# Optimization experiments

Hardware: AMD Instinct MI355X
Metric: run time of the kernel (lower is better)

Reference implementation:

```python
import jax, jax.numpy as jnp
import numpy as np


def setup_inputs() -> dict:
    key = jax.random.key(0)
    k1, k2 = jax.random.split(key)
    N, D, C = 8192, 512, 100
    e = jax.random.normal(k1, (N, D), dtype=jnp.float32)
    y = jax.random.randint(k2, (N,), 0, C, dtype=jnp.int64)
    return {"e": e, "y": y}


def reference(e, y):
    # L2-normalize rows (matches e / sqrt(sum(e*e, dim=1, keepdim=True)))
    e_norm = e / jnp.sqrt(jnp.sum(e * e, axis=1, keepdims=True))
    # Pairwise cosine similarities [N, N]
    sim = e_norm @ e_norm.T
    N = e.shape[0]
    # Pairs (i1, i2) with i1 < i2 and y[i1] != y[i2]
    upper = jnp.triu(jnp.ones((N, N), dtype=bool), k=1)
    diff_label = y[:, None] != y[None, :]
    mask = (upper & diff_label).astype(sim.dtype)
    cnter = jnp.sum(mask)
    loss = jnp.sum(sim * mask)
    return loss / cnter
```

## Files before the change

kernel.cpp:

```cpp
#include <hip/hip_runtime.h>
#include <hip/hip_bf16.h>

constexpr int N = 8192;
constexpr int D = 512;
constexpr int C = 100;
constexpr int CAP = 256;
constexpr int SLICES = 4;
constexpr int SLICE_D = D / SLICES;
constexpr int CHUNKS = 4;

constexpr size_t OFF_CLASSSUM = 512;
constexpr size_t OFF_INVN     = OFF_CLASSSUM + (size_t)C * D * 4;
constexpr size_t OFF_LIST     = OFF_INVN + (size_t)N * 4;
constexpr size_t ZERO_BYTES   = OFF_CLASSSUM + (size_t)C * D * 4;

__global__ __launch_bounds__(256) void norm_kernel(
    const float* __restrict__ e,
    const int* __restrict__ y,
    float* __restrict__ invn,
    int* __restrict__ counts,
    int* __restrict__ list) {
  const int row  = (blockIdx.x * 256 + threadIdx.x) >> 6;
  const int lane = threadIdx.x & 63;
  if (row >= N) return;

  const float4* ep = reinterpret_cast<const float4*>(e + (size_t)row * D);
  const float4 a = ep[lane];
  const float4 b = ep[lane + 64];
  float ss = a.x * a.x + a.y * a.y + a.z * a.z + a.w * a.w
           + b.x * b.x + b.y * b.y + b.z * b.z + b.w * b.w;
  #pragma unroll
  for (int off = 32; off > 0; off >>= 1) ss += __shfl_xor(ss, off);

  if (lane == 0) {
    invn[row] = 1.0f / sqrtf(ss);
    const int c = y[row];
    const int pos = atomicAdd(counts + c, 1);
    if (pos < CAP) list[c * CAP + pos] = row;
  }
}

__global__ __launch_bounds__(128) void gather_kernel(
    const float* __restrict__ e,
    const float* __restrict__ invn,
    const int* __restrict__ counts,
    const int* __restrict__ list,
    float* __restrict__ classSum) {
  const int c   = blockIdx.x / (SLICES * CHUNKS);
  const int s   = (blockIdx.x / CHUNKS) % SLICES;
  const int h   = blockIdx.x % CHUNKS;
  const int tid = threadIdx.x;

  int n = counts[c];
  if (n > CAP) n = CAP;
  const int per = (n + CHUNKS - 1) / CHUNKS;
  const int k0  = h * per;
  int k1 = k0 + per;
  if (k1 > n) k1 = n;
  const int m = k1 - k0;
  if (m <= 0) return;

  __shared__ int   ls[CAP / CHUNKS];
  __shared__ float li[CAP / CHUNKS];
  if (tid < m) {
    const int r = list[c * CAP + k0 + tid];
    ls[tid] = r;
    li[tid] = invn[r];
  }
  __syncthreads();

  float acc = 0.0f;
  const float* base = e + s * SLICE_D + tid;
  #pragma unroll 4
  for (int k = 0; k < m; ++k) {
    acc += base[(size_t)ls[k] * D] * li[k];
  }

  atomicAdd(classSum + c * D + s * SLICE_D + tid, acc);
}

__global__ __launch_bounds__(512) void final_kernel(
    const float* __restrict__ classSum,
    const int* __restrict__ counts,
    float* __restrict__ out) {
  const int d = threadIdx.x;
  float t = 0.0f, b = 0.0f;
  #pragma unroll 10
  for (int c = 0; c < C; ++c) {
    const float v = classSum[c * D + d];
    t += v;
    b += v * v;
  }
  __shared__ float shA[512];
  __shared__ float shB[512];
  __shared__ float shQ[512];
  shA[d] = t * t;
  shB[d] = b;
  if (d < C) {
    const float n = (float)counts[d];
    shQ[d] = n * n;
  } else {
    shQ[d] = 0.0f;
  }
  __syncthreads();
  for (int off = 256; off > 0; off >>= 1) {
    if (d < off) {
      shA[d] += shA[d + off];
      shB[d] += shB[d + off];
      shQ[d] += shQ[d + off];
    }
    __syncthreads();
  }
  if (d == 0) {
    const double A  = (double)shA[0];
    const double B  = (double)shB[0];
    const double sq = (double)shQ[0];
    out[0] = (float)((A - B) / ((double)N * (double)N - sq));
  }
}

extern "C" void kernel_launch(void* const* d_in, const int* in_sizes, int n_in,
                              void* d_out, int out_size, void* d_ws, size_t ws_size,
                              hipStream_t stream) {
  const float* e = (const float*)d_in[0];
  const int*   y = (const int*)d_in[1];
  float* out = (float*)d_out;

  char* ws = (char*)d_ws;
  int*   counts   = (int*)ws;
  float* classSum = (float*)(ws + OFF_CLASSSUM);
  float* invn     = (float*)(ws + OFF_INVN);
  int*   list     = (int*)(ws + OFF_LIST);

  hipMemsetAsync(d_ws, 0, ZERO_BYTES, stream);

  norm_kernel<<<N / 4, 256, 0, stream>>>(e, y, invn, counts, list);
  gather_kernel<<<C * SLICES * CHUNKS, 128, 0, stream>>>(e, invn, counts, list, classSum);
  final_kernel<<<1, 512, 0, stream>>>(classSum, counts, out);
}
```

Before: 100.5 us.

## Fuse final reduction into gather via last-block counter and zero classSum in norm

Merges the final reduction kernel into the gather kernel. An atomic done-counter picks the last finishing block, which then reads classSum and computes the scalar loss. The classSum zeroing moves from a large memset into norm_kernel, leaving only a small memset for counts and the counter. CHUNKS doubles to 8 for more gather parallelism. The aim is to remove one kernel launch and most of the memset cost, at the price of a serial tail in the single last block with only 128 threads, plus more atomics.

```diff
diff --git a/kernel.cpp b/kernel.cpp
--- a/kernel.cpp
+++ b/kernel.cpp
@@ -7,20 +7,24 @@
 constexpr int CAP = 256;
 constexpr int SLICES = 4;
 constexpr int SLICE_D = D / SLICES;
-constexpr int CHUNKS = 4;
+constexpr int CHUNKS = 8;
+constexpr int GBLOCKS = C * SLICES * CHUNKS;
 
 constexpr size_t OFF_CLASSSUM = 512;
 constexpr size_t OFF_INVN     = OFF_CLASSSUM + (size_t)C * D * 4;
 constexpr size_t OFF_LIST     = OFF_INVN + (size_t)N * 4;
-constexpr size_t ZERO_BYTES   = OFF_CLASSSUM + (size_t)C * D * 4;
 
 __global__ __launch_bounds__(256) void norm_kernel(
     const float* __restrict__ e,
     const int* __restrict__ y,
     float* __restrict__ invn,
     int* __restrict__ counts,
-    int* __restrict__ list) {
-  const int row  = (blockIdx.x * 256 + threadIdx.x) >> 6;
+    int* __restrict__ list,
+    float* __restrict__ classSum) {
+  const int gid  = blockIdx.x * 256 + threadIdx.x;
+  if (gid < C * D) classSum[gid] = 0.0f;
+
+  const int row  = gid >> 6;
   const int lane = threadIdx.x & 63;
   if (row >= N) return;
 
@@ -40,15 +44,18 @@
   }
 }
 
-__global__ __launch_bounds__(128) void gather_kernel(
+__global__ __launch_bounds__(128) void gather_final_kernel(
     const float* __restrict__ e,
     const float* __restrict__ invn,
     const int* __restrict__ counts,
     const int* __restrict__ list,
-    float* __restrict__ classSum) {
+    float* __restrict__ classSum,
+    int* __restrict__ done,
+    float* __restrict__ out) {
   const int c   = blockIdx.x / (SLICES * CHUNKS);
-  const int s   = (blockIdx.x / CHUNKS) % SLICES;
-  const int h   = blockIdx.x % CHUNKS;
+  const int rem = blockIdx.x % (SLICES * CHUNKS);
+  const int s   = rem / CHUNKS;
+  const int h   = rem % CHUNKS;
   const int tid = threadIdx.x;
 
   int n = counts[c];
@@ -58,63 +65,77 @@
   int k1 = k0 + per;
   if (k1 > n) k1 = n;
   const int m = k1 - k0;
-  if (m <= 0) return;
 
   __shared__ int   ls[CAP / CHUNKS];
   __shared__ float li[CAP / CHUNKS];
-  if (tid < m) {
-    const int r = list[c * CAP + k0 + tid];
-    ls[tid] = r;
-    li[tid] = invn[r];
+  if (m > 0) {
+    if (tid < m) {
+      const int r = list[c * CAP + k0 + tid];
+      ls[tid] = r;
+      li[tid] = invn[r];
+    }
+    __syncthreads();
+
+    float acc = 0.0f;
+    const float* base = e + s * SLICE_D + tid;
+    #pragma unroll 4
+    for (int k = 0; k < m; ++k) {
+      acc += base[(size_t)ls[k] * D] * li[k];
+    }
+    atomicAdd(classSum + c * D + s * SLICE_D + tid, acc);
+  }
+
+  __threadfence();
+  __syncthreads();
+  __shared__ int lastFlag;
+  if (tid == 0) {
+    const int old = atomicAdd(done, 1);
+    lastFlag = (old == GBLOCKS - 1) ? 1 : 0;
   }
   __syncthreads();
+  if (!lastFlag) return;
 
-  float acc = 0.0f;
-  const float* base = e + s * SLICE_D + tid;
-  #pragma unroll 4
-  for (int k = 0; k < m; ++k) {
-    acc += base[(size_t)ls[k] * D] * li[k];
+  __threadfence();
+  float Apart = 0.0f, Bpart = 0.0f;
+  #pragma unroll
+  for (int j = 0; j < 4; ++j) {
+    const int d = tid + 128 * j;
+    float t = 0.0f, b = 0.0f;
+    #pragma unroll 4
+    for (int c2 = 0; c2 < C; ++c2) {
+      const float v = __hip_atomic_load(classSum + c2 * D + d,
+                                        __ATOMIC_RELAXED, __HIP_MEMORY_SCOPE_AGENT);
+      t += v;
+      b += v * v;
+    }
+    Apart += t * t;
+    Bpart += b;
   }
+  #pragma unroll
+  for (int off = 32; off > 0; off >>= 1) {
+    Apart += __shfl_xor(Apart, off);
+    Bpart += __shfl_xor(Bpart, off);
+  }
+  int q = 0;
+  if (tid < C) {
+    const int nn = counts[tid];
+    q = nn * nn;
+  }
+  #pragma unroll
+  for (int off = 32; off > 0; off >>= 1) q += __shfl_xor(q, off);
 
-  atomicAdd(classSum + c * D + s * SLICE_D + tid, acc);
-}
-
-__global__ __launch_bounds__(512) void final_kernel(
-    const float* __restrict__ classSum,
-    const int* __restrict__ counts,
-    float* __restrict__ out) {
-  const int d = threadIdx.x;
-  float t = 0.0f, b = 0.0f;
-  #pragma unroll 10
-  for (int c = 0; c < C; ++c) {
-    const float v = classSum[c * D + d];
-    t += v;
-    b += v * v;
-  }
-  __shared__ float shA[512];
-  __shared__ float shB[512];
-  __shared__ float shQ[512];
-  shA[d] = t * t;
-  shB[d] = b;
-  if (d < C) {
-    const float n = (float)counts[d];
-    shQ[d] = n * n;
-  } else {
-    shQ[d] = 0.0f;
+  __shared__ float sA[2], sB[2];
+  __shared__ int   sQ[2];
+  if ((tid & 63) == 0) {
+    sA[tid >> 6] = Apart;
+    sB[tid >> 6] = Bpart;
+    sQ[tid >> 6] = q;
   }
   __syncthreads();
-  for (int off = 256; off > 0; off >>= 1) {
-    if (d < off) {
-      shA[d] += shA[d + off];
-      shB[d] += shB[d + off];
-      shQ[d] += shQ[d + off];
-    }
-    __syncthreads();
-  }
-  if (d == 0) {
-    const double A  = (double)shA[0];
-    const double B  = (double)shB[0];
-    const double sq = (double)shQ[0];
+  if (tid == 0) {
+    const double A  = (double)sA[0] + (double)sA[1];
+    const double B  = (double)sB[0] + (double)sB[1];
+    const double sq = (double)(sQ[0] + sQ[1]);
     out[0] = (float)((A - B) / ((double)N * (double)N - sq));
   }
 }
@@ -128,13 +149,14 @@
 
   char* ws = (char*)d_ws;
   int*   counts   = (int*)ws;
+  int*   done     = (int*)(ws + 400);
   float* classSum = (float*)(ws + OFF_CLASSSUM);
   float* invn     = (float*)(ws + OFF_INVN);
   int*   list     = (int*)(ws + OFF_LIST);
 
-  hipMemsetAsync(d_ws, 0, ZERO_BYTES, stream);
+  hipMemsetAsync(d_ws, 0, 512, stream);
 
-  norm_kernel<<<N / 4, 256, 0, stream>>>(e, y, invn, counts, list);
-  gather_kernel<<<C * SLICES * CHUNKS, 128, 0, stream>>>(e, invn, counts, list, classSum);
-  final_kernel<<<1, 512, 0, stream>>>(classSum, counts, out);
+  norm_kernel<<<N / 4, 256, 0, stream>>>(e, y, invn, counts, list, classSum);
+  gather_final_kernel<<<GBLOCKS, 128, 0, stream>>>(e, invn, counts, list,
+                                                   classSum, done, out);
 }
```

Measured after the change: 225.8 us. +124.6%, slower.
